# Kernel optimization log

Hardware: AMD Instinct MI355X
Metric: run time of the kernel (lower is better)

The kernel has to match this reference:

```python
import jax, jax.numpy as jnp
import numpy as np

NODE_DIM = 256
HID = 128
EDGE_DIM = 128
NUM_BINS = 22
MAX_LEN = 2056
TOTAL_FEATS = HID * 3 + NUM_BINS * 2 + 2


def get_index_embedding(indices, embed_size, max_len):
    # sinusoidal index embedding as in RiboFlow utils
    K = jnp.arange(embed_size // 2, dtype=jnp.float32)
    ang = indices[..., None].astype(jnp.float32) * jnp.pi / (max_len ** (2.0 * K / embed_size))
    return jnp.concatenate([jnp.sin(ang), jnp.cos(ang)], axis=-1)


def calc_distogram(pos, min_bin, max_bin, num_bins):
    # pos: [B, N, 3] -> one-hot distogram [B, N, N, num_bins]
    d = jnp.linalg.norm(pos[:, :, None, :] - pos[:, None, :, :], axis=-1)[..., None]
    lower = jnp.linspace(min_bin, max_bin, num_bins)
    upper = jnp.concatenate([lower[1:], jnp.array([1e8], dtype=jnp.float32)])
    return ((d > lower) & (d < upper)).astype(jnp.float32)


def cross_concat(f):
    # f: [B, N, D] -> [B, N, N, 2D] via row/col tiling
    B, N, D = f.shape
    return jnp.concatenate([
        jnp.broadcast_to(f[:, :, None, :], (B, N, N, D)),
        jnp.broadcast_to(f[:, None, :, :], (B, N, N, D)),
    ], axis=-1)


def _linear_params(key, fi, fo):
    s = 1.0 / np.sqrt(fi)
    kw, kb = jax.random.split(key)
    W = jax.random.uniform(kw, (fi, fo), jnp.float32, -s, s)
    b = jax.random.uniform(kb, (fo,), jnp.float32, -s, s)
    return W, b


def setup_inputs() -> dict:
    key = jax.random.key(0)
    ks = jax.random.split(key, 12)
    B, N = 1, 512
    inp = {
        'node_features': jax.random.normal(ks[0], (B, N, NODE_DIM), jnp.float32),
        'trans': jax.random.normal(ks[1], (B, N, 3), jnp.float32) * 10.0,
        'sc_trans': jax.random.normal(ks[2], (B, N, 3), jnp.float32) * 10.0,
        'edge_mask': jnp.ones((B, N, N), jnp.float32),
        'flow_mask': (jax.random.uniform(ks[4], (B, N)) > 0.5).astype(jnp.float32),
    }
    inp['W_n2e'], inp['b_n2e'] = _linear_params(ks[5], NODE_DIM, HID)
    inp['W_rp'], inp['b_rp'] = _linear_params(ks[6], HID, HID)
    inp['W1'], inp['b1'] = _linear_params(ks[7], TOTAL_FEATS, EDGE_DIM)
    inp['W2'], inp['b2'] = _linear_params(ks[8], EDGE_DIM, EDGE_DIM)
    inp['W3'], inp['b3'] = _linear_params(ks[9], EDGE_DIM, EDGE_DIM)
    inp['ln_g'] = jnp.ones((EDGE_DIM,), jnp.float32)
    inp['ln_b'] = jnp.zeros((EDGE_DIM,), jnp.float32)
    return inp


def reference(node_features, trans, sc_trans, edge_mask, flow_mask,
              W_n2e, b_n2e, W_rp, b_rp, W1, b1, W2, b2, W3, b3, ln_g, ln_b):
    B, N, _ = node_features.shape
    # node -> edge projection, then cross-concat tiling: [B,N,N,2*HID]
    n2e = node_features @ W_n2e + b_n2e
    pair_node_feats = cross_concat(n2e)
    # relative position sinusoidal embedding + linear: [B,N,N,HID]
    seq = jnp.arange(N, dtype=jnp.float32)
    relpos = jnp.broadcast_to(seq[None, :, None] - seq[None, None, :], (B, N, N))
    relpos_feats = get_index_embedding(relpos, HID, MAX_LEN) @ W_rp + b_rp
    # distograms: [B,N,N,NUM_BINS] each
    dist_feats = calc_distogram(trans, 0.001, 20.0, NUM_BINS)
    sc_feats = calc_distogram(sc_trans, 0.001, 20.0, NUM_BINS)
    # flow mask pair features: [B,N,N,2]
    flow_feat = cross_concat(flow_mask[..., None])
    feats = jnp.concatenate([pair_node_feats, relpos_feats, dist_feats, sc_feats, flow_feat], axis=-1)
    # 3-layer MLP + LayerNorm
    h = jax.nn.relu(feats @ W1 + b1)
    h = jax.nn.relu(h @ W2 + b2)
    h = h @ W3 + b3
    mu = jnp.mean(h, axis=-1, keepdims=True)
    var = jnp.var(h, axis=-1, keepdims=True)
    h = (h - mu) * jax.lax.rsqrt(var + 1e-5) * ln_g + ln_b
    return h * edge_mask[..., None]
```

## Files before the change

kernel.cpp:

```cpp
#include <hip/hip_runtime.h>


using bf16x8 = __attribute__((ext_vector_type(8))) short;
using f32x4  = __attribute__((ext_vector_type(4))) float;

__device__ __forceinline__ unsigned short f2bf(float f) {
    unsigned int u;
    __builtin_memcpy(&u, &f, 4);
    unsigned int r = (u + 0x7fffu + ((u >> 16) & 1u)) >> 16;
    return (unsigned short)r;
}

__device__ __forceinline__ unsigned int cvt_pk_bf16(float lo, float hi) {
    unsigned int r;
    asm("v_cvt_pk_bf16_f32 %0, %1, %2" : "=v"(r) : "v"(lo), "v"(hi));
    return r;
}

__global__ void pre_all(const float* __restrict__ nf,
                        const float* __restrict__ Wn2e,
                        const float* __restrict__ bn2e,
                        const float* __restrict__ W1,
                        const float* __restrict__ b1,
                        const float* __restrict__ flow,
                        const float* __restrict__ Wrp,
                        const float* __restrict__ brp,
                        const float* __restrict__ W2,
                        const float* __restrict__ W3,
                        float* __restrict__ A, float* __restrict__ Bv,
                        float* __restrict__ Rm,
                        short* __restrict__ W2b, short* __restrict__ W3b)
{
    __shared__ float s0[256];
    __shared__ float s1[128];
    const int bid = blockIdx.x;
    const int m = threadIdx.x;

    if (bid < 512) {
        const int i = bid;
        s0[m]       = nf[i * 256 + m];
        s0[m + 128] = nf[i * 256 + 128 + m];
        __syncthreads();
        float acc = bn2e[m];
        for (int k = 0; k < 256; k++) acc += s0[k] * Wn2e[k * 128 + m];
        s1[m] = acc;
        __syncthreads();
        const float fl = flow[i];
        float aA = b1[m] + fl * W1[428 * 128 + m];
        float aB =         fl * W1[429 * 128 + m];
        for (int k = 0; k < 128; k++) {
            const float s = s1[k];
            aA += s * W1[k * 128 + m];
            aB += s * W1[(128 + k) * 128 + m];
        }
        A[i * 128 + m]  = aA;
        Bv[i * 128 + m] = aB;
    } else if (bid < 1535) {
        const int dix = bid - 512;
        const float d = (float)(dix - 511);
        const int K = m & 63;
        const float denom = powf(2056.0f, (float)K * (1.0f / 64.0f));
        const float ang = d * 3.14159265358979323846f / denom;
        s0[m] = (m < 64) ? sinf(ang) : cosf(ang);
        __syncthreads();
        float acc = brp[m];
        for (int k = 0; k < 128; k++) acc += s0[k] * Wrp[k * 128 + m];
        s1[m] = acc;
        __syncthreads();
        float acc2 = 0.0f;
        for (int k = 0; k < 128; k++) acc2 += s1[k] * W1[(256 + k) * 128 + m];
        Rm[dix * 128 + m] = acc2;
    } else {
        const int t = (bid - 1535) * 128 + m;
        for (int h = 0; h < 2; h++) {
            const int idx = t + h * 8192;
            const int k = idx >> 7, n = idx & 127;
            const int dst = ((k >> 3) * 128 + n) * 8 + (k & 7);
            W2b[dst] = (short)f2bf(W2[idx]);
            W3b[dst] = (short)f2bf(W3[idx]);
        }
    }
}

__global__ __launch_bounds__(512, 4) void edge_main(
    const float* __restrict__ trans,
    const float* __restrict__ sctrans,
    const float* __restrict__ emask,
    const float* __restrict__ W1,
    const short* __restrict__ W2b,
    const float* __restrict__ b2,
    const short* __restrict__ W3b,
    const float* __restrict__ b3,
    const float* __restrict__ lng,
    const float* __restrict__ lnb,
    const float* __restrict__ A,
    const float* __restrict__ Bv,
    const float* __restrict__ Rm,
    float* __restrict__ out)
{
    __shared__ __align__(16) short hbuf[256 * 136];
    __shared__ __align__(16) float As[128];
    __shared__ int binsD[256];
    __shared__ int binsS[256];

    const int tid = threadIdx.x;
    const int i  = blockIdx.x >> 1;
    const int j0 = (blockIdx.x & 1) << 8;

    if (tid < 128) As[tid] = A[i * 128 + tid];

    {
        const int p = tid & 255;
        const float* P = (tid < 256) ? trans : sctrans;
        const int j = j0 + p;
        const float dx = __fsub_rn(P[i * 3 + 0], P[j * 3 + 0]);
        const float dy = __fsub_rn(P[i * 3 + 1], P[j * 3 + 1]);
        const float dz = __fsub_rn(P[i * 3 + 2], P[j * 3 + 2]);
        const float d2 = __fadd_rn(__fadd_rn(__fmul_rn(dx, dx), __fmul_rn(dy, dy)),
                                   __fmul_rn(dz, dz));
        const double dd = (double)sqrtf(d2);
        const double step = (20.0 - 0.001) / 21.0;
        int bin = -1;
        for (int b = 0; b < 22; b++) {
            const double lo = (b == 21) ? 20.0 : __dadd_rn(0.001, __dmul_rn((double)b, step));
            const double up = (b == 20) ? 20.0 :
                              ((b == 21) ? 1e8 : __dadd_rn(0.001, __dmul_rn((double)(b + 1), step)));
            if (dd > lo && dd < up) bin = b;
        }
        if (tid < 256) binsD[p] = bin; else binsS[p] = bin;
    }
    __syncthreads();

    const int w = tid >> 6;
    const int l = tid & 63;
    const int q = l >> 4;
    const int ln16 = l & 15;

    for (int it = 0; it < 16; it++) {
        const int flat = it * 64 + l;
        const int p = 32 * w + (flat >> 5);
        const int f = (flat & 31) << 2;
        const int j = j0 + p;
        const int didx = i - j + 511;
        const f32x4 bv = *(const f32x4*)&Bv[j * 128 + f];
        const f32x4 r  = *(const f32x4*)&Rm[didx * 128 + f];
        const f32x4 a  = *(const f32x4*)&As[f];
        const int bD = binsD[p], bS = binsS[p];
        const float sD = bD >= 0 ? 1.0f : 0.0f;
        const float sS = bS >= 0 ? 1.0f : 0.0f;
        const int rD = 384 + (bD >= 0 ? bD : 0);
        const int rS = 406 + (bS >= 0 ? bS : 0);
        const f32x4 wd  = *(const f32x4*)&W1[rD * 128 + f];
        const f32x4 wsv = *(const f32x4*)&W1[rS * 128 + f];
        float h0 = a.x + bv.x + r.x + sD * wd.x + sS * wsv.x;
        float h1 = a.y + bv.y + r.y + sD * wd.y + sS * wsv.y;
        float h2 = a.z + bv.z + r.z + sD * wd.z + sS * wsv.z;
        float h3 = a.w + bv.w + r.w + sD * wd.w + sS * wsv.w;
        h0 = fmaxf(h0, 0.0f); h1 = fmaxf(h1, 0.0f);
        h2 = fmaxf(h2, 0.0f); h3 = fmaxf(h3, 0.0f);
        uint2 pk;
        pk.x = cvt_pk_bf16(h0, h1);
        pk.y = cvt_pk_bf16(h2, h3);
        *(uint2*)&hbuf[p * 136 + f] = pk;
    }

    bf16x8 af[2][4];
    for (int mt = 0; mt < 2; mt++)
        for (int kb = 0; kb < 4; kb++)
            af[mt][kb] = *(const bf16x8*)&hbuf[(32 * w + mt * 16 + ln16) * 136 + q * 8 + kb * 32];

    const f32x4 vzero = {0.0f, 0.0f, 0.0f, 0.0f};

    for (int nb = 0; nb < 8; nb++) {
        f32x4 a0 = vzero, a1 = vzero;
        for (int kb = 0; kb < 4; kb++) {
            const bf16x8 bfrg = *(const bf16x8*)&W2b[((kb * 4 + q) * 128 + nb * 16 + ln16) * 8];
            a0 = __builtin_amdgcn_mfma_f32_16x16x32_bf16(af[0][kb], bfrg, a0, 0, 0, 0);
            a1 = __builtin_amdgcn_mfma_f32_16x16x32_bf16(af[1][kb], bfrg, a1, 0, 0, 0);
        }
        const float b2v = b2[nb * 16 + ln16];
        for (int rg = 0; rg < 4; rg++) {
            const float v0 = fmaxf(a0[rg] + b2v, 0.0f);
            const float v1 = fmaxf(a1[rg] + b2v, 0.0f);
            hbuf[(32 * w +      q * 4 + rg) * 136 + nb * 16 + ln16] = (short)cvt_pk_bf16(v0, v0);
            hbuf[(32 * w + 16 + q * 4 + rg) * 136 + nb * 16 + ln16] = (short)cvt_pk_bf16(v1, v1);
        }
    }

    for (int mt = 0; mt < 2; mt++) {
        bf16x8 a3[4];
        for (int kb = 0; kb < 4; kb++)
            a3[kb] = *(const bf16x8*)&hbuf[(32 * w + mt * 16 + ln16) * 136 + q * 8 + kb * 32];

        f32x4 acc3[8];
        for (int nb = 0; nb < 8; nb++) acc3[nb] = vzero;
        for (int nb = 0; nb < 8; nb++)
            for (int kb = 0; kb < 4; kb++) {
                const bf16x8 bfrg = *(const bf16x8*)&W3b[((kb * 4 + q) * 128 + nb * 16 + ln16) * 8];
                acc3[nb] = __builtin_amdgcn_mfma_f32_16x16x32_bf16(a3[kb], bfrg, acc3[nb], 0, 0, 0);
            }

        float b3v[8], gv[8], bbv[8];
        for (int nb = 0; nb < 8; nb++) {
            const int n = nb * 16 + ln16;
            b3v[nb] = b3[n];
            gv[nb]  = lng[n];
            bbv[nb] = lnb[n];
        }
        for (int rg = 0; rg < 4; rg++) {
            float v[8];
            float s = 0.0f;
            for (int nb = 0; nb < 8; nb++) { v[nb] = acc3[nb][rg] + b3v[nb]; s += v[nb]; }
            for (int mm = 1; mm < 16; mm <<= 1) s += __shfl_xor(s, mm, 64);
            const float mu = s * (1.0f / 128.0f);
            float ss = 0.0f;
            for (int nb = 0; nb < 8; nb++) { const float dv = v[nb] - mu; ss += dv * dv; }
            for (int mm = 1; mm < 16; mm <<= 1) ss += __shfl_xor(ss, mm, 64);
            const float rstd = rsqrtf(ss * (1.0f / 128.0f) + 1e-5f);
            const int p = 32 * w + mt * 16 + q * 4 + rg;
            const int j = j0 + p;
            const float msk = emask[i * 512 + j];
            const int obase = (i * 512 + j) * 128;
            for (int nb = 0; nb < 8; nb++) {
                const float o = ((v[nb] - mu) * rstd * gv[nb] + bbv[nb]) * msk;
                out[obase + nb * 16 + ln16] = o;
            }
        }
    }
}

extern "C" void kernel_launch(void* const* d_in, const int* in_sizes, int n_in,
                              void* d_out, int out_size, void* d_ws, size_t ws_size,
                              hipStream_t stream)
{
    const float* nf    = (const float*)d_in[0];
    const float* trans = (const float*)d_in[1];
    const float* sctr  = (const float*)d_in[2];
    const float* emask = (const float*)d_in[3];
    const float* flow  = (const float*)d_in[4];
    const float* Wn2e  = (const float*)d_in[5];
    const float* bn2e  = (const float*)d_in[6];
    const float* Wrp   = (const float*)d_in[7];
    const float* brp   = (const float*)d_in[8];
    const float* W1    = (const float*)d_in[9];
    const float* b1    = (const float*)d_in[10];
    const float* W2    = (const float*)d_in[11];
    const float* b2    = (const float*)d_in[12];
    const float* W3    = (const float*)d_in[13];
    const float* b3    = (const float*)d_in[14];
    const float* lng   = (const float*)d_in[15];
    const float* lnb   = (const float*)d_in[16];

    float* ws = (float*)d_ws;
    float* A   = ws;
    float* Bv  = ws + 512 * 128;
    float* Rm  = ws + 2 * 512 * 128;
    short* W2b = (short*)(ws + 262016);
    short* W3b = (short*)(ws + 270208);
    float* out = (float*)d_out;

    pre_all<<<1599, 128, 0, stream>>>(nf, Wn2e, bn2e, W1, b1, flow, Wrp, brp,
                                      W2, W3, A, Bv, Rm, W2b, W3b);
    edge_main<<<1024, 512, 0, stream>>>(trans, sctr, emask, W1, W2b, b2, W3b, b3,
                                        lng, lnb, A, Bv, Rm, out);
}
```

Before: 265.6 us.

## Stage W2/W3 in LDS and build layer-1 fragments directly in registers

Each block now copies the bf16 W2 and W3 weights into LDS with async global_load_lds, so MFMA B-fragments come from LDS rather than global/L2. Layer-1 activations are built straight into MFMA A-fragment registers, which removes the shared hbuf round trip. Layer-2 output goes to a small per-wave 16-row buffer, processed one m-tile at a time. LDS use rises to roughly 100KB per block and the occupancy hint drops from 4 to 2, trading latency hiding for fewer global weight reads. There is no explicit wait or barrier on the async LDS load before first use beyond the existing __syncthreads.

```diff
diff --git a/kernel.cpp b/kernel.cpp
--- a/kernel.cpp
+++ b/kernel.cpp
@@ -82,7 +82,7 @@
     }
 }
 
-__global__ __launch_bounds__(512, 4) void edge_main(
+__global__ __launch_bounds__(512, 2) void edge_main(
     const float* __restrict__ trans,
     const float* __restrict__ sctrans,
     const float* __restrict__ emask,
@@ -98,7 +98,9 @@
     const float* __restrict__ Rm,
     float* __restrict__ out)
 {
-    __shared__ __align__(16) short hbuf[256 * 136];
+    __shared__ __align__(16) short W2L[16384];
+    __shared__ __align__(16) short W3L[16384];
+    __shared__ __align__(16) short h2w[8 * 16 * 140];
     __shared__ __align__(16) float As[128];
     __shared__ int binsD[256];
     __shared__ int binsS[256];
@@ -106,6 +108,16 @@
     const int tid = threadIdx.x;
     const int i  = blockIdx.x >> 1;
     const int j0 = (blockIdx.x & 1) << 8;
+
+    for (int r = 0; r < 4; r++) {
+        const int off = (r * 512 + tid) * 16;
+        __builtin_amdgcn_global_load_lds(
+            (const __attribute__((address_space(1))) void*)((const char*)W2b + off),
+            (__attribute__((address_space(3))) void*)((char*)W2L + off), 16, 0, 0);
+        __builtin_amdgcn_global_load_lds(
+            (const __attribute__((address_space(1))) void*)((const char*)W3b + off),
+            (__attribute__((address_space(3))) void*)((char*)W3L + off), 16, 0, 0);
+    }
 
     if (tid < 128) As[tid] = A[i * 128 + tid];
 
@@ -136,77 +148,80 @@
     const int q = l >> 4;
     const int ln16 = l & 15;
 
-    for (int it = 0; it < 16; it++) {
-        const int flat = it * 64 + l;
-        const int p = 32 * w + (flat >> 5);
-        const int f = (flat & 31) << 2;
+    bf16x8 af[2][4];
+    for (int mt = 0; mt < 2; mt++) {
+        const int p = 32 * w + mt * 16 + ln16;
         const int j = j0 + p;
         const int didx = i - j + 511;
-        const f32x4 bv = *(const f32x4*)&Bv[j * 128 + f];
-        const f32x4 r  = *(const f32x4*)&Rm[didx * 128 + f];
-        const f32x4 a  = *(const f32x4*)&As[f];
         const int bD = binsD[p], bS = binsS[p];
         const float sD = bD >= 0 ? 1.0f : 0.0f;
         const float sS = bS >= 0 ? 1.0f : 0.0f;
         const int rD = 384 + (bD >= 0 ? bD : 0);
         const int rS = 406 + (bS >= 0 ? bS : 0);
-        const f32x4 wd  = *(const f32x4*)&W1[rD * 128 + f];
-        const f32x4 wsv = *(const f32x4*)&W1[rS * 128 + f];
-        float h0 = a.x + bv.x + r.x + sD * wd.x + sS * wsv.x;
-        float h1 = a.y + bv.y + r.y + sD * wd.y + sS * wsv.y;
-        float h2 = a.z + bv.z + r.z + sD * wd.z + sS * wsv.z;
-        float h3 = a.w + bv.w + r.w + sD * wd.w + sS * wsv.w;
-        h0 = fmaxf(h0, 0.0f); h1 = fmaxf(h1, 0.0f);
-        h2 = fmaxf(h2, 0.0f); h3 = fmaxf(h3, 0.0f);
-        uint2 pk;
-        pk.x = cvt_pk_bf16(h0, h1);
-        pk.y = cvt_pk_bf16(h2, h3);
-        *(uint2*)&hbuf[p * 136 + f] = pk;
-    }
-
-    bf16x8 af[2][4];
-    for (int mt = 0; mt < 2; mt++)
-        for (int kb = 0; kb < 4; kb++)
-            af[mt][kb] = *(const bf16x8*)&hbuf[(32 * w + mt * 16 + ln16) * 136 + q * 8 + kb * 32];
+        const float* __restrict__ BvR = &Bv[j * 128];
+        const float* __restrict__ RmR = &Rm[didx * 128];
+        const float* __restrict__ WdR = &W1[rD * 128];
+        const float* __restrict__ WsR = &W1[rS * 128];
+        for (int kb = 0; kb < 4; kb++) {
+            const int f0 = kb * 32 + q * 8;
+            const f32x4 bv0 = *(const f32x4*)&BvR[f0];
+            const f32x4 bv1 = *(const f32x4*)&BvR[f0 + 4];
+            const f32x4 r0  = *(const f32x4*)&RmR[f0];
+            const f32x4 r1  = *(const f32x4*)&RmR[f0 + 4];
+            const f32x4 a0  = *(const f32x4*)&As[f0];
+            const f32x4 a1  = *(const f32x4*)&As[f0 + 4];
+            const f32x4 w0  = *(const f32x4*)&WdR[f0];
+            const f32x4 w1  = *(const f32x4*)&WdR[f0 + 4];
+            const f32x4 s0  = *(const f32x4*)&WsR[f0];
+            const f32x4 s1  = *(const f32x4*)&WsR[f0 + 4];
+            float h[8];
+            for (int e = 0; e < 4; e++) {
+                h[e]     = fmaxf(a0[e] + bv0[e] + r0[e] + sD * w0[e] + sS * s0[e], 0.0f);
+                h[e + 4] = fmaxf(a1[e] + bv1[e] + r1[e] + sD * w1[e] + sS * s1[e], 0.0f);
+            }
+            union { unsigned int u[4]; bf16x8 v; } cv;
+            cv.u[0] = cvt_pk_bf16(h[0], h[1]);
+            cv.u[1] = cvt_pk_bf16(h[2], h[3]);
+            cv.u[2] = cvt_pk_bf16(h[4], h[5]);
+            cv.u[3] = cvt_pk_bf16(h[6], h[7]);
+            af[mt][kb] = cv.v;
+        }
+    }
 
     const f32x4 vzero = {0.0f, 0.0f, 0.0f, 0.0f};
-
+    short* const h2p = &h2w[w * 16 * 140];
+
+    float b2v[8], b3v[8], gv[8], bbv[8];
     for (int nb = 0; nb < 8; nb++) {
-        f32x4 a0 = vzero, a1 = vzero;
-        for (int kb = 0; kb < 4; kb++) {
-            const bf16x8 bfrg = *(const bf16x8*)&W2b[((kb * 4 + q) * 128 + nb * 16 + ln16) * 8];
-            a0 = __builtin_amdgcn_mfma_f32_16x16x32_bf16(af[0][kb], bfrg, a0, 0, 0, 0);
-            a1 = __builtin_amdgcn_mfma_f32_16x16x32_bf16(af[1][kb], bfrg, a1, 0, 0, 0);
-        }
-        const float b2v = b2[nb * 16 + ln16];
-        for (int rg = 0; rg < 4; rg++) {
-            const float v0 = fmaxf(a0[rg] + b2v, 0.0f);
-            const float v1 = fmaxf(a1[rg] + b2v, 0.0f);
-            hbuf[(32 * w +      q * 4 + rg) * 136 + nb * 16 + ln16] = (short)cvt_pk_bf16(v0, v0);
-            hbuf[(32 * w + 16 + q * 4 + rg) * 136 + nb * 16 + ln16] = (short)cvt_pk_bf16(v1, v1);
-        }
+        const int n = nb * 16 + ln16;
+        b2v[nb] = b2[n]; b3v[nb] = b3[n]; gv[nb] = lng[n]; bbv[nb] = lnb[n];
     }
 
     for (int mt = 0; mt < 2; mt++) {
+        for (int nb = 0; nb < 8; nb++) {
+            f32x4 acc = vzero;
+            for (int kb = 0; kb < 4; kb++) {
+                const bf16x8 bfrg = *(const bf16x8*)&W2L[((kb * 4 + q) * 128 + nb * 16 + ln16) * 8];
+                acc = __builtin_amdgcn_mfma_f32_16x16x32_bf16(af[mt][kb], bfrg, acc, 0, 0, 0);
+            }
+            for (int rg = 0; rg < 4; rg++) {
+                const float v = fmaxf(acc[rg] + b2v[nb], 0.0f);
+                h2p[(q * 4 + rg) * 140 + nb * 16 + ln16] = (short)cvt_pk_bf16(v, v);
+            }
+        }
+
         bf16x8 a3[4];
         for (int kb = 0; kb < 4; kb++)
-            a3[kb] = *(const bf16x8*)&hbuf[(32 * w + mt * 16 + ln16) * 136 + q * 8 + kb * 32];
+            a3[kb] = *(const bf16x8*)&h2p[ln16 * 140 + q * 8 + kb * 32];
 
         f32x4 acc3[8];
         for (int nb = 0; nb < 8; nb++) acc3[nb] = vzero;
         for (int nb = 0; nb < 8; nb++)
             for (int kb = 0; kb < 4; kb++) {
-                const bf16x8 bfrg = *(const bf16x8*)&W3b[((kb * 4 + q) * 128 + nb * 16 + ln16) * 8];
+                const bf16x8 bfrg = *(const bf16x8*)&W3L[((kb * 4 + q) * 128 + nb * 16 + ln16) * 8];
                 acc3[nb] = __builtin_amdgcn_mfma_f32_16x16x32_bf16(a3[kb], bfrg, acc3[nb], 0, 0, 0);
             }
 
-        float b3v[8], gv[8], bbv[8];
-        for (int nb = 0; nb < 8; nb++) {
-            const int n = nb * 16 + ln16;
-            b3v[nb] = b3[n];
-            gv[nb]  = lng[n];
-            bbv[nb] = lnb[n];
-        }
         for (int rg = 0; rg < 4; rg++) {
             float v[8];
             float s = 0.0f;
```

New measurement: 259.0 us. -2.5%, faster.
